# Optimization experiments

Hardware: AMD Instinct MI355X
Metric: run time of the kernel (lower is better)

Reference implementation:

```python
import jax, jax.numpy as jnp
import numpy as np

N, E, B = 100000, 1600000, 512
NE, EE, H = 32, 32, 64
SCALE = float(2**48 - 1)


def _mlp2(x, W1, b1, W2, b2):
    # Linear -> ReLU -> Linear
    return jax.nn.relu(x @ W1 + b1) @ W2 + b2


def _gine(x, src, dst, e, W1, b1, W2, b2, n):
    # GINEConv (eps=0): nn(x + sum_j relu(x_j + e_ij))
    m = jax.nn.relu(x[src] + e)                      # [E, d] gather + edge add
    agg = jax.ops.segment_sum(m, dst, num_segments=n)  # scatter-add to targets
    return _mlp2(x + agg, W1, b1, W2, b2)


def _encode(names, edge_index, edge_attr, batch,
            idW1, idb1, idW2, idb2, edW1, edb1, edW2, edb2,
            c1W1, c1b1, c1W2, c1b2, c2W1, c2b1, c2W2, c2b2, linW, linb):
    norm = jnp.clip((names.astype(jnp.float32) + 2.0) / SCALE, 0.0, 1.0)[:, None]
    x = _mlp2(norm, idW1, idb1, idW2, idb2)          # [N, NE]
    e = _mlp2(edge_attr, edW1, edb1, edW2, edb2)     # [E, EE]
    src, dst = edge_index[0], edge_index[1]
    x = jax.nn.relu(_gine(x, src, dst, e, c1W1, c1b1, c1W2, c1b2, N))
    e2 = e @ linW + linb                             # edge lin for conv2 (EE->H)
    x = jax.nn.relu(_gine(x, src, dst, e2, c2W1, c2b1, c2W2, c2b2, N))
    sums = jax.ops.segment_sum(x, batch, num_segments=B)
    cnt = jax.ops.segment_sum(jnp.ones((x.shape[0],), x.dtype), batch, num_segments=B)
    return sums / jnp.maximum(cnt, 1.0)[:, None]     # global_mean_pool


def setup_inputs() -> dict:
    key = jax.random.key(0)
    ks = iter(jax.random.split(key, 64))
    def w(shape):
        return jax.random.normal(next(ks), shape, dtype=jnp.float32) * 0.05
    d = {}
    d['node_names_s'] = jax.random.randint(next(ks), (N,), 0, 1000000)
    d['edge_index_s'] = jax.random.randint(next(ks), (2, E), 0, N)
    d['edge_attr_s'] = jax.random.uniform(next(ks), (E, 1), dtype=jnp.float32)
    d['batch_s'] = jnp.sort(jax.random.randint(next(ks), (N,), 0, B))
    d['node_names_g'] = jax.random.randint(next(ks), (N,), 0, 1000000)
    d['edge_index_g'] = jax.random.randint(next(ks), (2, E), 0, N)
    d['edge_attr_g'] = jax.random.uniform(next(ks), (E, 1), dtype=jnp.float32)
    d['batch_g'] = jnp.sort(jax.random.randint(next(ks), (N,), 0, B))
    d['depth'] = jax.random.uniform(next(ks), (B,), dtype=jnp.float32)
    # shared encoders
    d['idW1'], d['idb1'], d['idW2'], d['idb2'] = w((1, NE)), w((NE,)), w((NE, NE)), w((NE,))
    d['edW1'], d['edb1'], d['edW2'], d['edb2'] = w((1, EE)), w((EE,)), w((EE, EE)), w((EE,))
    # state convs
    d['s1W1'], d['s1b1'], d['s1W2'], d['s1b2'] = w((NE, H)), w((H,)), w((H, H)), w((H,))
    d['s2W1'], d['s2b1'], d['s2W2'], d['s2b2'] = w((H, H)), w((H,)), w((H, H)), w((H,))
    d['s2linW'], d['s2linb'] = w((EE, H)), w((H,))
    # goal convs
    d['g1W1'], d['g1b1'], d['g1W2'], d['g1b2'] = w((NE, H)), w((H,)), w((H, H)), w((H,))
    d['g2W1'], d['g2b1'], d['g2W2'], d['g2b2'] = w((H, H)), w((H,)), w((H, H)), w((H,))
    d['g2linW'], d['g2linb'] = w((EE, H)), w((H,))
    d['rW1'], d['rb1'], d['rW2'], d['rb2'] = w((2 * H + 1, H)), w((H,)), w((H, 1)), w((1,))
    return d


def reference(node_names_s, edge_index_s, edge_attr_s, batch_s,
              node_names_g, edge_index_g, edge_attr_g, batch_g, depth,
              idW1, idb1, idW2, idb2, edW1, edb1, edW2, edb2,
              s1W1, s1b1, s1W2, s1b2, s2W1, s2b1, s2W2, s2b2, s2linW, s2linb,
              g1W1, g1b1, g1W2, g1b2, g2W1, g2b1, g2W2, g2b2, g2linW, g2linb,
              rW1, rb1, rW2, rb2):
    s = _encode(node_names_s, edge_index_s, edge_attr_s, batch_s,
                idW1, idb1, idW2, idb2, edW1, edb1, edW2, edb2,
                s1W1, s1b1, s1W2, s1b2, s2W1, s2b1, s2W2, s2b2, s2linW, s2linb)
    g = _encode(node_names_g, edge_index_g, edge_attr_g, batch_g,
                idW1, idb1, idW2, idb2, edW1, edb1, edW2, edb2,
                g1W1, g1b1, g1W2, g1b2, g2W1, g2b1, g2W2, g2b2, g2linW, g2linb)
    z = jnp.concatenate([s, g, depth[:, None]], axis=1)  # [B, 2H+1]
    return _mlp2(z, rW1, rb1, rW2, rb2)[:, 0]            # [B]
```

## Files before the change

kernel.cpp:

```cpp
#include <hip/hip_runtime.h>
#include <hip/hip_fp16.h>
#include <stdint.h>

namespace {

constexpr int NN   = 100000;
constexpr int TN   = 2 * NN;
constexpr int NEDG = 1600000;
constexpr int TE   = 2 * NEDG;
constexpr int NBAT = 512;
constexpr int NSEG = 33;

constexpr int NC     = 782;
constexpr int TILE   = 4096;
constexpr int ABLK   = (TE + TILE - 1) / TILE;
constexpr int ENTCAP = 5120;

constexpr int S1H = 20;
constexpr int S2H = 36;

constexpr int TAB_BP = 0;
constexpr int TAB_D1 = 32;
constexpr int TAB_C1 = TAB_D1 + NSEG * 32;
constexpr int TAB_E2 = TAB_C1 + NSEG * 32;
constexpr int TAB_TOTAL = TAB_E2 + 4 * NSEG * 64;

__device__ __forceinline__ float relu_(float x) { return fmaxf(x, 0.0f); }

__device__ __forceinline__ float4 shfl_xor4(float4 v, int m) {
  return make_float4(__shfl_xor(v.x, m), __shfl_xor(v.y, m),
                     __shfl_xor(v.z, m), __shfl_xor(v.w, m));
}

__device__ __forceinline__ __half2 bch(int u) {
  return *reinterpret_cast<__half2*>(&u);
}
__device__ __forceinline__ int f2h2(float a, float b) {
  __half2 h = __floats2half2_rn(a, b);
  return *reinterpret_cast<int*>(&h);
}

__global__ void build_tables(const float* __restrict__ eW1, const float* __restrict__ eb1,
                             const float* __restrict__ eW2, const float* __restrict__ eb2,
                             const float* __restrict__ sLW, const float* __restrict__ sLb,
                             const float* __restrict__ gLW, const float* __restrict__ gLb,
                             float* __restrict__ tabs) {
  __shared__ float traw[32];
  __shared__ float ts[32];
  __shared__ float dt[NSEG * 32];
  __shared__ float ct[NSEG * 32];
  int tid = threadIdx.x;
  if (tid < 32) {
    float w = eW1[tid], b = eb1[tid];
    traw[tid] = (w != 0.0f) ? (-b / w) : 3.0e38f;
  }
  __syncthreads();
  if (tid < 32) {
    float v = traw[tid];
    int r = 0;
    for (int j = 0; j < 32; ++j) {
      float u = traw[j];
      r += (u < v) || (u == v && j < tid);
    }
    ts[r] = v;
  }
  __syncthreads();
  if (tid < 32) tabs[TAB_BP + tid] = ts[tid];
  for (int idx = tid; idx < NSEG * 32; idx += blockDim.x) {
    int s = idx >> 5, j = idx & 31;
    float a;
    if (s == 0)            a = ts[0] - 1.0f;
    else if (s == NSEG - 1) a = ts[31] + 1.0f;
    else                   a = 0.5f * ts[s - 1] + 0.5f * ts[s];
    float d = 0.0f, c = 0.0f;
    for (int i = 0; i < 32; ++i) {
      float w = eW1[i], b = eb1[i];
      if (fmaf(a, w, b) > 0.0f) {
        float w2 = eW2[i * 32 + j];
        d = fmaf(w, w2, d);
        c = fmaf(b, w2, c);
      }
    }
    c += eb2[j];
    dt[idx] = d; ct[idx] = c;
    tabs[TAB_D1 + idx] = d;
    tabs[TAB_C1 + idx] = c;
  }
  __syncthreads();
  for (int idx = tid; idx < NSEG * 64; idx += blockDim.x) {
    int s = idx >> 6, k = idx & 63;
    float ds = 0.f, cs = 0.f, dg = 0.f, cg = 0.f;
    for (int j = 0; j < 32; ++j) {
      float dv = dt[s * 32 + j], cv = ct[s * 32 + j];
      float ws = sLW[j * 64 + k], wg = gLW[j * 64 + k];
      ds = fmaf(dv, ws, ds); cs = fmaf(cv, ws, cs);
      dg = fmaf(dv, wg, dg); cg = fmaf(cv, wg, cg);
    }
    cs += sLb[k]; cg += gLb[k];
    tabs[TAB_E2 + idx]                 = ds;
    tabs[TAB_E2 + NSEG * 64 + idx]     = cs;
    tabs[TAB_E2 + 2 * NSEG * 64 + idx] = dg;
    tabs[TAB_E2 + 3 * NSEG * 64 + idx] = cg;
  }
}

__global__ __launch_bounds__(256) void fused_front(
    const int* __restrict__ names_s, const int* __restrict__ names_g,
    const float* __restrict__ idW1, const float* __restrict__ idb1,
    const float* __restrict__ idW2, const float* __restrict__ idb2,
    const int* __restrict__ src_s, const int* __restrict__ dst_s, const float* __restrict__ attr_s,
    const int* __restrict__ src_g, const int* __restrict__ dst_g, const float* __restrict__ attr_g,
    const int* __restrict__ bat_s, const int* __restrict__ bat_g,
    const float* __restrict__ tabs,
    float* __restrict__ x0, __half* __restrict__ x0h,
    int* __restrict__ gcur, int2* __restrict__ part,
    int* __restrict__ start_s, int* __restrict__ start_g) {
  __shared__ int hist[NC];
  __shared__ int lofs[NC];
  __shared__ int lcur[NC];
  __shared__ int2 sorted[TILE];
  __shared__ int addr[TILE];
  __shared__ int scanbuf[256];
  __shared__ float bp[32];
  int t = threadIdx.x;
  if (blockIdx.x < ABLK) {
    if (t < 32) bp[t] = tabs[TAB_BP + t];
    for (int i = t; i < NC; i += 256) hist[i] = 0;
    __syncthreads();
    int base = blockIdx.x * TILE;
#pragma unroll
    for (int j = 0; j < 16; ++j) {
      int i = base + j * 256 + t;
      if (i < TE) {
        int d = (i < NEDG) ? dst_s[i] : (dst_g[i - NEDG] + NN);
        atomicAdd(&hist[d >> 8], 1);
      }
    }
    __syncthreads();
    int loc[4];
    int sum = 0;
#pragma unroll
    for (int j = 0; j < 4; ++j) {
      int b = t * 4 + j;
      int v = (b < NC) ? hist[b] : 0;
      loc[j] = sum; sum += v;
    }
    scanbuf[t] = sum;
    __syncthreads();
    for (int st = 1; st < 256; st <<= 1) {
      int u = (t >= st) ? scanbuf[t - st] : 0;
      __syncthreads();
      scanbuf[t] += u;
      __syncthreads();
    }
    int texcl = scanbuf[t] - sum;
#pragma unroll
    for (int j = 0; j < 4; ++j) {
      int b = t * 4 + j;
      if (b < NC) { lofs[b] = texcl + loc[j]; lcur[b] = 0; }
    }
    __syncthreads();
    for (int b = t; b < NC; b += 256) {
      int c = hist[b];
      hist[b] = c ? atomicAdd(&gcur[b], c) : 0;
    }
    __syncthreads();
#pragma unroll
    for (int j = 0; j < 16; ++j) {
      int i = base + j * 256 + t;
      if (i < TE) {
        int sl, d; float a;
        if (i < NEDG) { sl = src_s[i]; d = dst_s[i]; a = attr_s[i]; }
        else { int k = i - NEDG; sl = src_g[k]; d = dst_g[k] + NN; a = attr_g[k]; }
        int seg = 0;
#pragma unroll
        for (int q = 0; q < 32; ++q) seg += (bp[q] < a);
        int c = d >> 8;
        int r = atomicAdd(&lcur[c], 1);
        int s = lofs[c] + r;
        sorted[s] = make_int2(sl | ((d & 255) << 17) | (seg << 25), __float_as_int(a));
        addr[s] = c * ENTCAP + hist[c] + r;
      }
    }
    __syncthreads();
    int tot = (base + TILE <= TE) ? TILE : (TE - base);
    for (int s = t; s < tot; s += 256) part[addr[s]] = sorted[s];
  } else if (blockIdx.x < ABLK + 782) {
    int n = (blockIdx.x - ABLK) * 256 + t;
    if (n >= TN) return;
    int name = (n < NN) ? names_s[n] : names_g[n - NN];
    float norm = ((float)name + 2.0f) / 281474976710655.0f;
    norm = fminf(fmaxf(norm, 0.0f), 1.0f);
    float h[32];
#pragma unroll
    for (int i = 0; i < 32; ++i) h[i] = relu_(fmaf(norm, idW1[i], idb1[i]));
    float4* out = (float4*)(x0 + (size_t)n * 32);
    int2* outh = (int2*)(x0h + (size_t)n * 32);
    for (int j0 = 0; j0 < 32; j0 += 4) {
      float a0 = idb2[j0], a1 = idb2[j0 + 1], a2 = idb2[j0 + 2], a3 = idb2[j0 + 3];
#pragma unroll
      for (int i = 0; i < 32; ++i) {
        float hv = h[i];
        a0 = fmaf(hv, idW2[i * 32 + j0],     a0);
        a1 = fmaf(hv, idW2[i * 32 + j0 + 1], a1);
        a2 = fmaf(hv, idW2[i * 32 + j0 + 2], a2);
        a3 = fmaf(hv, idW2[i * 32 + j0 + 3], a3);
      }
      out[j0 >> 2] = make_float4(a0, a1, a2, a3);
      outh[j0 >> 2] = make_int2(f2h2(a0, a1), f2h2(a2, a3));
    }
  } else {
    int blk = blockIdx.x - ABLK - 782;
    int half = blk >= 391;
    const int* bat = half ? bat_g : bat_s;
    int* start = half ? start_g : start_s;
    int i = (blk - half * 391) * 256 + t;
    if (i >= NN) return;
    int cur = bat[i];
    int prev = (i == 0) ? -1 : bat[i - 1];
    for (int b = prev + 1; b <= cur; ++b) start[b] = i;
    if (i == NN - 1) {
      for (int b = cur + 1; b <= NBAT; ++b) start[b] = NN;
    }
  }
}

__global__ __launch_bounds__(1024) void coarse_scan(
    const int* __restrict__ gcur, int* __restrict__ cbase, int* __restrict__ rowptr) {
  __shared__ int s[1024];
  int t = threadIdx.x;
  int v = (t < NC) ? min(gcur[t], ENTCAP) : 0;
  s[t] = v;
  __syncthreads();
  for (int st = 1; st < 1024; st <<= 1) {
    int u = (t >= st) ? s[t - st] : 0;
    __syncthreads();
    s[t] += u;
    __syncthreads();
  }
  if (t < NC) cbase[t] = s[t] - v;
  if (t == 0) rowptr[TN] = TE;
}

__global__ __launch_bounds__(256) void partition_to_csr(
    const int* __restrict__ gcur, const int* __restrict__ cbase,
    const int2* __restrict__ part,
    int* __restrict__ rowptr, int2* __restrict__ colattr) {
  __shared__ int2 outE[ENTCAP];
  __shared__ int hist[256];
  __shared__ int cur[256];
  __shared__ int sc[256];
  int t = threadIdx.x, b = blockIdx.x;
  hist[t] = 0;
  __syncthreads();
  int cnt = min(gcur[b], ENTCAP);
  int ibase = b * ENTCAP;
  int obase = cbase[b];
  for (int i = t; i < cnt; i += 256)
    atomicAdd(&hist[(part[ibase + i].x >> 17) & 255], 1);
  __syncthreads();
  int v = hist[t];
  sc[t] = v;
  __syncthreads();
  for (int st = 1; st < 256; st <<= 1) {
    int u = (t >= st) ? sc[t - st] : 0;
    __syncthreads();
    sc[t] += u;
    __syncthreads();
  }
  int excl = sc[t] - v;
  int gnode = b * 256 + t;
  if (gnode < TN) rowptr[gnode] = obase + excl;
  cur[t] = excl;
  __syncthreads();
  for (int i = t; i < cnt; i += 256) {
    int2 e = part[ibase + i];
    int dl = (e.x >> 17) & 255;
    int srcn = e.x & 0x1FFFF;
    int seg = (e.x >> 25) & 63;
    int pos = atomicAdd(&cur[dl], 1);
    outE[pos] = make_int2(srcn | (seg << 20), e.y);
  }
  __syncthreads();
  for (int i = t; i < cnt; i += 256) colattr[obase + i] = outE[i];
}

__global__ __launch_bounds__(256) void conv1_dual(
    const float* __restrict__ x0, const __half* __restrict__ x0h,
    const int* __restrict__ rowptr, const int2* __restrict__ colattr,
    const float* __restrict__ tabs, float* __restrict__ hb) {
  __shared__ __half2 dt2[NSEG * S1H];
  __shared__ __half2 ct2[NSEG * S1H];
  for (int i = threadIdx.x; i < NSEG * 16; i += 256) {
    int s = i >> 4, j = i & 15;
    dt2[s * S1H + j] = __floats2half2_rn(tabs[TAB_D1 + s * 32 + 2 * j],
                                         tabs[TAB_D1 + s * 32 + 2 * j + 1]);
    ct2[s * S1H + j] = __floats2half2_rn(tabs[TAB_C1 + s * 32 + 2 * j],
                                         tabs[TAB_C1 + s * 32 + 2 * j + 1]);
  }
  __syncthreads();
  int n = blockIdx.x * 4 + (threadIdx.x >> 6);
  const __half* xb = x0h + (n >= NN ? (size_t)NN * 32 : 0);
  int lane = threadIdx.x & 63;
  int sub = lane & 7;
  int f0  = (lane >> 3) * 4;
  int h0  = (lane >> 3) * 2;
  int beg = rowptr[n], end = rowptr[n + 1];
  float4 acc = make_float4(0.f, 0.f, 0.f, 0.f);
  for (int k = beg + sub; k < end; k += 16) {
    int2 ca0 = colattr[k];
    int kb = k + 8;
    bool has1 = kb < end;
    int2 ca1 = has1 ? colattr[kb] : ca0;
    unsigned p0 = (unsigned)ca0.x, p1 = (unsigned)ca1.x;
    int s0 = (int)(p0 & 0xFFFFFu), g0 = (int)(p0 >> 20);
    int s1 = (int)(p1 & 0xFFFFFu), g1 = (int)(p1 >> 20);
    float a0 = __int_as_float(ca0.y), a1 = __int_as_float(ca1.y);
    __half2 az0 = __floats2half2_rn(a0, a0);
    __half2 az1 = __floats2half2_rn(a1, a1);
    int2 xv0 = *(const int2*)(xb + (size_t)s0 * 32 + f0);
    int2 xv1 = *(const int2*)(xb + (size_t)s1 * 32 + f0);
    int2 dv0 = *(const int2*)&dt2[g0 * S1H + h0];
    int2 cv0 = *(const int2*)&ct2[g0 * S1H + h0];
    __half2 v;
    float2 f;
    v = __hadd2(bch(xv0.x), __hfma2(az0, bch(dv0.x), bch(cv0.x)));
    f = __half22float2(v); acc.x += relu_(f.x); acc.y += relu_(f.y);
    v = __hadd2(bch(xv0.y), __hfma2(az0, bch(dv0.y), bch(cv0.y)));
    f = __half22float2(v); acc.z += relu_(f.x); acc.w += relu_(f.y);
    if (has1) {
      int2 dv1 = *(const int2*)&dt2[g1 * S1H + h0];
      int2 cv1 = *(const int2*)&ct2[g1 * S1H + h0];
      v = __hadd2(bch(xv1.x), __hfma2(az1, bch(dv1.x), bch(cv1.x)));
      f = __half22float2(v); acc.x += relu_(f.x); acc.y += relu_(f.y);
      v = __hadd2(bch(xv1.y), __hfma2(az1, bch(dv1.y), bch(cv1.y)));
      f = __half22float2(v); acc.z += relu_(f.x); acc.w += relu_(f.y);
    }
  }
#pragma unroll
  for (int m = 1; m < 8; m <<= 1) {
    float4 o = shfl_xor4(acc, m);
    acc.x += o.x; acc.y += o.y; acc.z += o.z; acc.w += o.w;
  }
  if (sub == 0) {
    const float4 self = *(const float4*)(x0 + (size_t)n * 32 + f0);
    *(float4*)(hb + (size_t)n * 32 + f0) =
        make_float4(self.x + acc.x, self.y + acc.y, self.z + acc.z, self.w + acc.w);
  }
}

__global__ __launch_bounds__(256) void conv2_dual(
    const float* __restrict__ x1, const __half* __restrict__ x1h,
    const int* __restrict__ rowptr, const int2* __restrict__ colattr,
    const float* __restrict__ tabs, float* __restrict__ hb) {
  __shared__ __half2 dt2[NSEG * S2H];
  __shared__ __half2 ct2[NSEG * S2H];
  int half = blockIdx.x >= (NN / 4);
  const float* d2 = tabs + TAB_E2 + (size_t)half * 2 * NSEG * 64;
  for (int i = threadIdx.x; i < NSEG * 32; i += 256) {
    int s = i >> 5, j = i & 31;
    dt2[s * S2H + j] = __floats2half2_rn(d2[s * 64 + 2 * j], d2[s * 64 + 2 * j + 1]);
    ct2[s * S2H + j] = __floats2half2_rn(d2[NSEG * 64 + s * 64 + 2 * j],
                                         d2[NSEG * 64 + s * 64 + 2 * j + 1]);
  }
  __syncthreads();
  int n = blockIdx.x * 4 + (threadIdx.x >> 6);
  const __half* xb = x1h + (size_t)half * NN * 64;
  int lane = threadIdx.x & 63;
  int sub = lane & 7;
  int f0  = (lane >> 3) * 8;
  int h0  = (lane >> 3) * 4;
  int beg = rowptr[n], end = rowptr[n + 1];
  float4 accA = make_float4(0.f, 0.f, 0.f, 0.f);
  float4 accB = make_float4(0.f, 0.f, 0.f, 0.f);
  for (int k = beg + sub; k < end; k += 16) {
    int2 ca0 = colattr[k];
    int kb = k + 8;
    bool has1 = kb < end;
    int2 ca1 = has1 ? colattr[kb] : ca0;
    unsigned p0 = (unsigned)ca0.x, p1 = (unsigned)ca1.x;
    int s0 = (int)(p0 & 0xFFFFFu), g0 = (int)(p0 >> 20);
    int s1 = (int)(p1 & 0xFFFFFu), g1 = (int)(p1 >> 20);
    float a0 = __int_as_float(ca0.y), a1 = __int_as_float(ca1.y);
    __half2 az0 = __floats2half2_rn(a0, a0);
    __half2 az1 = __floats2half2_rn(a1, a1);
    int4 xv0 = *(const int4*)(xb + (size_t)s0 * 64 + f0);
    int4 xv1 = *(const int4*)(xb + (size_t)s1 * 64 + f0);
    int4 dv0 = *(const int4*)&dt2[g0 * S2H + h0];
    int4 cv0 = *(const int4*)&ct2[g0 * S2H + h0];
    __half2 v;
    float2 f;
    v = __hadd2(bch(xv0.x), __hfma2(az0, bch(dv0.x), bch(cv0.x)));
    f = __half22float2(v); accA.x += relu_(f.x); accA.y += relu_(f.y);
    v = __hadd2(bch(xv0.y), __hfma2(az0, bch(dv0.y), bch(cv0.y)));
    f = __half22float2(v); accA.z += relu_(f.x); accA.w += relu_(f.y);
    v = __hadd2(bch(xv0.z), __hfma2(az0, bch(dv0.z), bch(cv0.z)));
    f = __half22float2(v); accB.x += relu_(f.x); accB.y += relu_(f.y);
    v = __hadd2(bch(xv0.w), __hfma2(az0, bch(dv0.w), bch(cv0.w)));
    f = __half22float2(v); accB.z += relu_(f.x); accB.w += relu_(f.y);
    if (has1) {
      int4 dv1 = *(const int4*)&dt2[g1 * S2H + h0];
      int4 cv1 = *(const int4*)&ct2[g1 * S2H + h0];
      v = __hadd2(bch(xv1.x), __hfma2(az1, bch(dv1.x), bch(cv1.x)));
      f = __half22float2(v); accA.x += relu_(f.x); accA.y += relu_(f.y);
      v = __hadd2(bch(xv1.y), __hfma2(az1, bch(dv1.y), bch(cv1.y)));
      f = __half22float2(v); accA.z += relu_(f.x); accA.w += relu_(f.y);
      v = __hadd2(bch(xv1.z), __hfma2(az1, bch(dv1.z), bch(cv1.z)));
      f = __half22float2(v); accB.x += relu_(f.x); accB.y += relu_(f.y);
      v = __hadd2(bch(xv1.w), __hfma2(az1, bch(dv1.w), bch(cv1.w)));
      f = __half22float2(v); accB.z += relu_(f.x); accB.w += relu_(f.y);
    }
  }
#pragma unroll
  for (int m = 1; m < 8; m <<= 1) {
    float4 oA = shfl_xor4(accA, m);
    float4 oB = shfl_xor4(accB, m);
    accA.x += oA.x; accA.y += oA.y; accA.z += oA.z; accA.w += oA.w;
    accB.x += oB.x; accB.y += oB.y; accB.z += oB.z; accB.w += oB.w;
  }
  if (sub == 0) {
    const float* sp = x1 + (size_t)n * 64 + f0;
    const float4 sA = *(const float4*)sp;
    const float4 sB = *(const float4*)(sp + 4);
    float* op = hb + (size_t)n * 64 + f0;
    *(float4*)op       = make_float4(sA.x + accA.x, sA.y + accA.y, sA.z + accA.z, sA.w + accA.w);
    *(float4*)(op + 4) = make_float4(sB.x + accB.x, sB.y + accB.y, sB.z + accB.z, sB.w + accB.w);
  }
}

__global__ __launch_bounds__(256) void mlp1_dual(
    const float* __restrict__ hin,
    const float* __restrict__ sW1, const float* __restrict__ sb1,
    const float* __restrict__ sW2, const float* __restrict__ sb2,
    const float* __restrict__ gW1, const float* __restrict__ gb1,
    const float* __restrict__ gW2, const float* __restrict__ gb2,
    float* __restrict__ xout, __half* __restrict__ hout) {
  constexpr int IN = 32;
  __shared__ float hsT[IN][65];
  __shared__ float ysT[64][65];
  int base = blockIdx.x * 64;
  for (int idx = threadIdx.x; idx < 64 * IN; idx += 256) {
    int node = idx / IN, k = idx - node * IN;
    hsT[k][node] = hin[(size_t)(base + node) * IN + k];
  }
  __syncthreads();
  int nt = threadIdx.x >> 4, jx = threadIdx.x & 15;
  int n0 = nt * 4, f0 = jx * 4;
  bool isg = (base + n0) >= NN;
  const float* W1 = isg ? gW1 : sW1;
  const float* b1 = isg ? gb1 : sb1;
  const float* W2 = isg ? gW2 : sW2;
  const float* b2 = isg ? gb2 : sb2;
  float4 acc0, acc1, acc2, acc3;
  {
    const float4 b = *(const float4*)(b1 + f0);
    acc0 = b; acc1 = b; acc2 = b; acc3 = b;
  }
  for (int k = 0; k < IN; ++k) {
    const float4 h = *(const float4*)&hsT[k][n0];
    const float4 w = *(const float4*)(W1 + k * 64 + f0);
    acc0.x = fmaf(h.x, w.x, acc0.x); acc0.y = fmaf(h.x, w.y, acc0.y);
    acc0.z = fmaf(h.x, w.z, acc0.z); acc0.w = fmaf(h.x, w.w, acc0.w);
    acc1.x = fmaf(h.y, w.x, acc1.x); acc1.y = fmaf(h.y, w.y, acc1.y);
    acc1.z = fmaf(h.y, w.z, acc1.z); acc1.w = fmaf(h.y, w.w, acc1.w);
    acc2.x = fmaf(h.z, w.x, acc2.x); acc2.y = fmaf(h.z, w.y, acc2.y);
    acc2.z = fmaf(h.z, w.z, acc2.z); acc2.w = fmaf(h.z, w.w, acc2.w);
    acc3.x = fmaf(h.w, w.x, acc3.x); acc3.y = fmaf(h.w, w.y, acc3.y);
    acc3.z = fmaf(h.w, w.z, acc3.z); acc3.w = fmaf(h.w, w.w, acc3.w);
  }
  ysT[f0 + 0][n0 + 0] = relu_(acc0.x); ysT[f0 + 1][n0 + 0] = relu_(acc0.y);
  ysT[f0 + 2][n0 + 0] = relu_(acc0.z); ysT[f0 + 3][n0 + 0] = relu_(acc0.w);
  ysT[f0 + 0][n0 + 1] = relu_(acc1.x); ysT[f0 + 1][n0 + 1] = relu_(acc1.y);
  ysT[f0 + 2][n0 + 1] = relu_(acc1.z); ysT[f0 + 3][n0 + 1] = relu_(acc1.w);
  ysT[f0 + 0][n0 + 2] = relu_(acc2.x); ysT[f0 + 1][n0 + 2] = relu_(acc2.y);
  ysT[f0 + 2][n0 + 2] = relu_(acc2.z); ysT[f0 + 3][n0 + 2] = relu_(acc2.w);
  ysT[f0 + 0][n0 + 3] = relu_(acc3.x); ysT[f0 + 1][n0 + 3] = relu_(acc3.y);
  ysT[f0 + 2][n0 + 3] = relu_(acc3.z); ysT[f0 + 3][n0 + 3] = relu_(acc3.w);
  __syncthreads();
  {
    const float4 b = *(const float4*)(b2 + f0);
    acc0 = b; acc1 = b; acc2 = b; acc3 = b;
  }
  for (int k = 0; k < 64; ++k) {
    const float4 h = *(const float4*)&ysT[k][n0];
    const float4 w = *(const float4*)(W2 + k * 64 + f0);
    acc0.x = fmaf(h.x, w.x, acc0.x); acc0.y = fmaf(h.x, w.y, acc0.y);
    acc0.z = fmaf(h.x, w.z, acc0.z); acc0.w = fmaf(h.x, w.w, acc0.w);
    acc1.x = fmaf(h.y, w.x, acc1.x); acc1.y = fmaf(h.y, w.y, acc1.y);
    acc1.z = fmaf(h.y, w.z, acc1.z); acc1.w = fmaf(h.y, w.w, acc1.w);
    acc2.x = fmaf(h.z, w.x, acc2.x); acc2.y = fmaf(h.z, w.y, acc2.y);
    acc2.z = fmaf(h.z, w.z, acc2.z); acc2.w = fmaf(h.z, w.w, acc2.w);
    acc3.x = fmaf(h.w, w.x, acc3.x); acc3.y = fmaf(h.w, w.y, acc3.y);
    acc3.z = fmaf(h.w, w.z, acc3.z); acc3.w = fmaf(h.w, w.w, acc3.w);
  }
  float4 o;
  o = make_float4(relu_(acc0.x), relu_(acc0.y), relu_(acc0.z), relu_(acc0.w));
  *(float4*)(xout + (size_t)(base + n0 + 0) * 64 + f0) = o;
  *(int2*)(hout + (size_t)(base + n0 + 0) * 64 + f0) = make_int2(f2h2(o.x, o.y), f2h2(o.z, o.w));
  o = make_float4(relu_(acc1.x), relu_(acc1.y), relu_(acc1.z), relu_(acc1.w));
  *(float4*)(xout + (size_t)(base + n0 + 1) * 64 + f0) = o;
  *(int2*)(hout + (size_t)(base + n0 + 1) * 64 + f0) = make_int2(f2h2(o.x, o.y), f2h2(o.z, o.w));
  o = make_float4(relu_(acc2.x), relu_(acc2.y), relu_(acc2.z), relu_(acc2.w));
  *(float4*)(xout + (size_t)(base + n0 + 2) * 64 + f0) = o;
  *(int2*)(hout + (size_t)(base + n0 + 2) * 64 + f0) = make_int2(f2h2(o.x, o.y), f2h2(o.z, o.w));
  o = make_float4(relu_(acc3.x), relu_(acc3.y), relu_(acc3.z), relu_(acc3.w));
  *(float4*)(xout + (size_t)(base + n0 + 3) * 64 + f0) = o;
  *(int2*)(hout + (size_t)(base + n0 + 3) * 64 + f0) = make_int2(f2h2(o.x, o.y), f2h2(o.z, o.w));
}

__global__ __launch_bounds__(256) void mlp2_pool_dual(
    const float* __restrict__ hin,
    const float* __restrict__ sW1, const float* __restrict__ sb1,
    const float* __restrict__ sW2, const float* __restrict__ sb2,
    const float* __restrict__ gW1, const float* __restrict__ gb1,
    const float* __restrict__ gW2, const float* __restrict__ gb2,
    const int* __restrict__ bat_s, const int* __restrict__ bat_g,
    float* __restrict__ psum) {
  constexpr int IN = 64;
  __shared__ float hsT[IN][65];
  __shared__ float ysT[64][65];
  __shared__ int pid[64];
  int base = blockIdx.x * 64;
  for (int idx = threadIdx.x; idx < 64 * IN; idx += 256) {
    int node = idx / IN, k = idx - node * IN;
    hsT[k][node] = hin[(size_t)(base + node) * IN + k];
  }
  if (threadIdx.x < 64) {
    int gb = base + threadIdx.x;
    pid[threadIdx.x] = (gb < NN) ? bat_s[gb] : (NBAT + bat_g[gb - NN]);
  }
  __syncthreads();
  int nt = threadIdx.x >> 4, jx = threadIdx.x & 15;
  int n0 = nt * 4, f0 = jx * 4;
  bool isg = (base + n0) >= NN;
  const float* W1 = isg ? gW1 : sW1;
  const float* b1 = isg ? gb1 : sb1;
  const float* W2 = isg ? gW2 : sW2;
  const float* b2 = isg ? gb2 : sb2;
  float4 acc0, acc1, acc2, acc3;
  {
    const float4 b = *(const float4*)(b1 + f0);
    acc0 = b; acc1 = b; acc2 = b; acc3 = b;
  }
  for (int k = 0; k < IN; ++k) {
    const float4 h = *(const float4*)&hsT[k][n0];
    const float4 w = *(const float4*)(W1 + k * 64 + f0);
    acc0.x = fmaf(h.x, w.x, acc0.x); acc0.y = fmaf(h.x, w.y, acc0.y);
    acc0.z = fmaf(h.x, w.z, acc0.z); acc0.w = fmaf(h.x, w.w, acc0.w);
    acc1.x = fmaf(h.y, w.x, acc1.x); acc1.y = fmaf(h.y, w.y, acc1.y);
    acc1.z = fmaf(h.y, w.z, acc1.z); acc1.w = fmaf(h.y, w.w, acc1.w);
    acc2.x = fmaf(h.z, w.x, acc2.x); acc2.y = fmaf(h.z, w.y, acc2.y);
    acc2.z = fmaf(h.z, w.z, acc2.z); acc2.w = fmaf(h.z, w.w, acc2.w);
    acc3.x = fmaf(h.w, w.x, acc3.x); acc3.y = fmaf(h.w, w.y, acc3.y);
    acc3.z = fmaf(h.w, w.z, acc3.z); acc3.w = fmaf(h.w, w.w, acc3.w);
  }
  ysT[f0 + 0][n0 + 0] = relu_(acc0.x); ysT[f0 + 1][n0 + 0] = relu_(acc0.y);
  ysT[f0 + 2][n0 + 0] = relu_(acc0.z); ysT[f0 + 3][n0 + 0] = relu_(acc0.w);
  ysT[f0 + 0][n0 + 1] = relu_(acc1.x); ysT[f0 + 1][n0 + 1] = relu_(acc1.y);
  ysT[f0 + 2][n0 + 1] = relu_(acc1.z); ysT[f0 + 3][n0 + 1] = relu_(acc1.w);
  ysT[f0 + 0][n0 + 2] = relu_(acc2.x); ysT[f0 + 1][n0 + 2] = relu_(acc2.y);
  ysT[f0 + 2][n0 + 2] = relu_(acc2.z); ysT[f0 + 3][n0 + 2] = relu_(acc2.w);
  ysT[f0 + 0][n0 + 3] = relu_(acc3.x); ysT[f0 + 1][n0 + 3] = relu_(acc3.y);
  ysT[f0 + 2][n0 + 3] = relu_(acc3.z); ysT[f0 + 3][n0 + 3] = relu_(acc3.w);
  __syncthreads();
  {
    const float4 b = *(const float4*)(b2 + f0);
    acc0 = b; acc1 = b; acc2 = b; acc3 = b;
  }
  for (int k = 0; k < 64; ++k) {
    const float4 h = *(const float4*)&ysT[k][n0];
    const float4 w = *(const float4*)(W2 + k * 64 + f0);
    acc0.x = fmaf(h.x, w.x, acc0.x); acc0.y = fmaf(h.x, w.y, acc0.y);
    acc0.z = fmaf(h.x, w.z, acc0.z); acc0.w = fmaf(h.x, w.w, acc0.w);
    acc1.x = fmaf(h.y, w.x, acc1.x); acc1.y = fmaf(h.y, w.y, acc1.y);
    acc1.z = fmaf(h.y, w.z, acc1.z); acc1.w = fmaf(h.y, w.w, acc1.w);
    acc2.x = fmaf(h.z, w.x, acc2.x); acc2.y = fmaf(h.z, w.y, acc2.y);
    acc2.z = fmaf(h.z, w.z, acc2.z); acc2.w = fmaf(h.z, w.w, acc2.w);
    acc3.x = fmaf(h.w, w.x, acc3.x); acc3.y = fmaf(h.w, w.y, acc3.y);
    acc3.z = fmaf(h.w, w.z, acc3.z); acc3.w = fmaf(h.w, w.w, acc3.w);
  }
  __syncthreads();
  ysT[f0 + 0][n0 + 0] = relu_(acc0.x); ysT[f0 + 1][n0 + 0] = relu_(acc0.y);
  ysT[f0 + 2][n0 + 0] = relu_(acc0.z); ysT[f0 + 3][n0 + 0] = relu_(acc0.w);
  ysT[f0 + 0][n0 + 1] = relu_(acc1.x); ysT[f0 + 1][n0 + 1] = relu_(acc1.y);
  ysT[f0 + 2][n0 + 1] = relu_(acc1.z); ysT[f0 + 3][n0 + 1] = relu_(acc1.w);
  ysT[f0 + 0][n0 + 2] = relu_(acc2.x); ysT[f0 + 1][n0 + 2] = relu_(acc2.y);
  ysT[f0 + 2][n0 + 2] = relu_(acc2.z); ysT[f0 + 3][n0 + 2] = relu_(acc2.w);
  ysT[f0 + 0][n0 + 3] = relu_(acc3.x); ysT[f0 + 1][n0 + 3] = relu_(acc3.y);
  ysT[f0 + 2][n0 + 3] = relu_(acc3.z); ysT[f0 + 3][n0 + 3] = relu_(acc3.w);
  __syncthreads();
  int c = threadIdx.x >> 6, f = threadIdx.x & 63;
  int cur = pid[c * 16];
  float run = 0.0f;
  for (int i = 0; i < 16; ++i) {
    int nx = c * 16 + i;
    int p = pid[nx];
    if (p != cur) { atomicAdd(&psum[(size_t)cur * 64 + f], run); run = 0.0f; cur = p; }
    run += ysT[f][nx];
  }
  atomicAdd(&psum[(size_t)cur * 64 + f], run);
}

__global__ __launch_bounds__(256) void regressor16(
    const float* __restrict__ psum,
    const int* __restrict__ start_s, const int* __restrict__ start_g,
    const float* __restrict__ depth,
    const float* __restrict__ W1, const float* __restrict__ b1,
    const float* __restrict__ W2, const float* __restrict__ b2,
    float* __restrict__ out) {
  __shared__ float zs[16][132];
  __shared__ float ys[64][17];
  __shared__ float inv_s[16], inv_g[16];
  int base = blockIdx.x * 16;
  if (threadIdx.x < 16) {
    int b = base + threadIdx.x;
    inv_s[threadIdx.x] = 1.0f / fmaxf((float)(start_s[b + 1] - start_s[b]), 1.0f);
    inv_g[threadIdx.x] = 1.0f / fmaxf((float)(start_g[b + 1] - start_g[b]), 1.0f);
  }
  __syncthreads();
  for (int i = threadIdx.x; i < 16 * 64; i += 256) {
    int ln = i >> 6, k = i & 63;
    zs[ln][k]      = psum[(size_t)(base + ln) * 64 + k] * inv_s[ln];
    zs[ln][64 + k] = psum[(size_t)(NBAT + base + ln) * 64 + k] * inv_g[ln];
  }
  if (threadIdx.x < 16) zs[threadIdx.x][128] = depth[base + threadIdx.x];
  __syncthreads();
  int g = threadIdx.x >> 4;
  int j = threadIdx.x & 15;
  int f0 = j * 4;
  float a0, a1, a2, a3;
  {
    const float4 b = *(const float4*)(b1 + f0);
    a0 = b.x; a1 = b.y; a2 = b.z; a3 = b.w;
  }
  for (int k = 0; k < 129; ++k) {
    float zv = zs[g][k];
    const float4 w = *(const float4*)(W1 + k * 64 + f0);
    a0 = fmaf(zv, w.x, a0); a1 = fmaf(zv, w.y, a1);
    a2 = fmaf(zv, w.z, a2); a3 = fmaf(zv, w.w, a3);
  }
  ys[f0 + 0][g] = relu_(a0);
  ys[f0 + 1][g] = relu_(a1);
  ys[f0 + 2][g] = relu_(a2);
  ys[f0 + 3][g] = relu_(a3);
  __syncthreads();
  float s = ys[f0 + 0][g] * W2[f0 + 0] + ys[f0 + 1][g] * W2[f0 + 1] +
            ys[f0 + 2][g] * W2[f0 + 2] + ys[f0 + 3][g] * W2[f0 + 3];
#pragma unroll
  for (int m = 1; m < 16; m <<= 1) s += __shfl_xor(s, m);
  if (j == 0) out[base + g] = s + b2[0];
}

}

extern "C" void kernel_launch(void* const* d_in, const int* in_sizes, int n_in,
                              void* d_out, int out_size, void* d_ws, size_t ws_size,
                              hipStream_t stream) {
  const int*   names_s = (const int*)d_in[0];
  const int*   ei_s    = (const int*)d_in[1];
  const float* ea_s    = (const float*)d_in[2];
  const int*   bat_s   = (const int*)d_in[3];
  const int*   names_g = (const int*)d_in[4];
  const int*   ei_g    = (const int*)d_in[5];
  const float* ea_g    = (const float*)d_in[6];
  const int*   bat_g   = (const int*)d_in[7];
  const float* depth   = (const float*)d_in[8];
  const float* idW1 = (const float*)d_in[9],  *idb1 = (const float*)d_in[10];
  const float* idW2 = (const float*)d_in[11], *idb2 = (const float*)d_in[12];
  const float* edW1 = (const float*)d_in[13], *edb1 = (const float*)d_in[14];
  const float* edW2 = (const float*)d_in[15], *edb2 = (const float*)d_in[16];
  const float* s1W1 = (const float*)d_in[17], *s1b1 = (const float*)d_in[18];
  const float* s1W2 = (const float*)d_in[19], *s1b2 = (const float*)d_in[20];
  const float* s2W1 = (const float*)d_in[21], *s2b1 = (const float*)d_in[22];
  const float* s2W2 = (const float*)d_in[23], *s2b2 = (const float*)d_in[24];
  const float* s2LW = (const float*)d_in[25], *s2Lb = (const float*)d_in[26];
  const float* g1W1 = (const float*)d_in[27], *g1b1 = (const float*)d_in[28];
  const float* g1W2 = (const float*)d_in[29], *g1b2 = (const float*)d_in[30];
  const float* g2W1 = (const float*)d_in[31], *g2b1 = (const float*)d_in[32];
  const float* g2W2 = (const float*)d_in[33], *g2b2 = (const float*)d_in[34];
  const float* g2LW = (const float*)d_in[35], *g2Lb = (const float*)d_in[36];
  const float* rW1  = (const float*)d_in[37], *rb1  = (const float*)d_in[38];
  const float* rW2  = (const float*)d_in[39], *rb2  = (const float*)d_in[40];
  (void)in_sizes; (void)n_in; (void)out_size; (void)ws_size;

  char* ws = (char*)d_ws;
  size_t off = 0;
  auto alloc = [&](size_t bytes) -> char* {
    char* p = ws + off;
    off += (bytes + 255) & ~(size_t)255;
    return p;
  };
  float* tabs    = (float*)alloc((size_t)TAB_TOTAL * 4);
  char*  act   = alloc((size_t)TN * 64 * 4 * 2);
  float* x0buf = (float*)act;
  float* h1buf = (float*)(act + (size_t)TN * 32 * 4);
  float* x1buf = (float*)(act + (size_t)TN * 64 * 4);
  int2*  part  = (int2*)x1buf;
  float* h2buf = (float*)act;
  __half* x0h  = (__half*)alloc((size_t)TN * 32 * 2);
  __half* x1h  = (__half*)alloc((size_t)TN * 64 * 2);
  int2*  colattr = (int2*) alloc((size_t)TE * 8);
  int*   gcur    = (int*)  alloc((size_t)NC * 4);
  int*   cbase   = (int*)  alloc((size_t)NC * 4);
  int*   rowptr  = (int*)  alloc((size_t)(TN + 1) * 4);
  int*   start_s = (int*)  alloc((size_t)(NBAT + 1) * 4);
  int*   start_g = (int*)  alloc((size_t)(NBAT + 1) * 4);
  float* psum    = (float*)alloc((size_t)2 * NBAT * 64 * 4);

  build_tables<<<1, 256, 0, stream>>>(edW1, edb1, edW2, edb2, s2LW, s2Lb, g2LW, g2Lb, tabs);
  hipMemsetAsync(gcur, 0, (size_t)NC * 4, stream);
  hipMemsetAsync(psum, 0, (size_t)2 * NBAT * 64 * 4, stream);

  fused_front<<<ABLK + 782 + 782, 256, 0, stream>>>(
      names_s, names_g, idW1, idb1, idW2, idb2,
      ei_s, ei_s + NEDG, ea_s, ei_g, ei_g + NEDG, ea_g,
      bat_s, bat_g, tabs, x0buf, x0h, gcur, part, start_s, start_g);
  coarse_scan<<<1, 1024, 0, stream>>>(gcur, cbase, rowptr);
  partition_to_csr<<<NC, 256, 0, stream>>>(gcur, cbase, part, rowptr, colattr);

  conv1_dual<<<TN / 4, 256, 0, stream>>>(x0buf, x0h, rowptr, colattr, tabs, h1buf);
  mlp1_dual<<<TN / 64, 256, 0, stream>>>(h1buf,
                                         s1W1, s1b1, s1W2, s1b2,
                                         g1W1, g1b1, g1W2, g1b2, x1buf, x1h);
  conv2_dual<<<TN / 4, 256, 0, stream>>>(x1buf, x1h, rowptr, colattr, tabs, h2buf);
  mlp2_pool_dual<<<TN / 64, 256, 0, stream>>>(h2buf,
                                              s2W1, s2b1, s2W2, s2b2,
                                              g2W1, g2b1, g2W2, g2b2,
                                              bat_s, bat_g, psum);
  regressor16<<<32, 256, 0, stream>>>(psum, start_s, start_g, depth,
                                      rW1, rb1, rW2, rb2, (float*)d_out);
}
```

Measured before the change: 678.1 us.

## Drop fp32 node feature copies and make conv kernels persistent with rowptr prefetch

Removes the fp32 copies of x0 and x1 so only the fp16 versions are written, and the self term in each conv is read from the half buffer. conv1/conv2 now launch a fixed grid of 2048 blocks that grid-stride over nodes, loading the edge tables into shared memory once per block and prefetching the next node's rowptr. This cuts global write and read traffic and per-block table setup, at the cost of rounding the self term to fp16 and possible load imbalance from the fixed grid. Workspace is also reshuffled so the partition buffer aliases h2buf.

```diff
diff --git a/kernel.cpp b/kernel.cpp
--- a/kernel.cpp
+++ b/kernel.cpp
@@ -15,6 +15,8 @@
 constexpr int TILE   = 4096;
 constexpr int ABLK   = (TE + TILE - 1) / TILE;
 constexpr int ENTCAP = 5120;
+
+constexpr int CONVBLK = 2048;
 
 constexpr int S1H = 20;
 constexpr int S2H = 36;
@@ -112,7 +114,7 @@
     const int* __restrict__ src_g, const int* __restrict__ dst_g, const float* __restrict__ attr_g,
     const int* __restrict__ bat_s, const int* __restrict__ bat_g,
     const float* __restrict__ tabs,
-    float* __restrict__ x0, __half* __restrict__ x0h,
+    __half* __restrict__ x0h,
     int* __restrict__ gcur, int2* __restrict__ part,
     int* __restrict__ start_s, int* __restrict__ start_g) {
   __shared__ int hist[NC];
@@ -194,7 +196,6 @@
     float h[32];
 #pragma unroll
     for (int i = 0; i < 32; ++i) h[i] = relu_(fmaf(norm, idW1[i], idb1[i]));
-    float4* out = (float4*)(x0 + (size_t)n * 32);
     int2* outh = (int2*)(x0h + (size_t)n * 32);
     for (int j0 = 0; j0 < 32; j0 += 4) {
       float a0 = idb2[j0], a1 = idb2[j0 + 1], a2 = idb2[j0 + 2], a3 = idb2[j0 + 3];
@@ -206,7 +207,6 @@
         a2 = fmaf(hv, idW2[i * 32 + j0 + 2], a2);
         a3 = fmaf(hv, idW2[i * 32 + j0 + 3], a3);
       }
-      out[j0 >> 2] = make_float4(a0, a1, a2, a3);
       outh[j0 >> 2] = make_int2(f2h2(a0, a1), f2h2(a2, a3));
     }
   } else {
@@ -286,7 +286,7 @@
 }
 
 __global__ __launch_bounds__(256) void conv1_dual(
-    const float* __restrict__ x0, const __half* __restrict__ x0h,
+    const __half* __restrict__ x0h,
     const int* __restrict__ rowptr, const int2* __restrict__ colattr,
     const float* __restrict__ tabs, float* __restrict__ hb) {
   __shared__ __half2 dt2[NSEG * S1H];
@@ -299,64 +299,71 @@
                                          tabs[TAB_C1 + s * 32 + 2 * j + 1]);
   }
   __syncthreads();
-  int n = blockIdx.x * 4 + (threadIdx.x >> 6);
-  const __half* xb = x0h + (n >= NN ? (size_t)NN * 32 : 0);
   int lane = threadIdx.x & 63;
   int sub = lane & 7;
   int f0  = (lane >> 3) * 4;
   int h0  = (lane >> 3) * 2;
-  int beg = rowptr[n], end = rowptr[n + 1];
-  float4 acc = make_float4(0.f, 0.f, 0.f, 0.f);
-  for (int k = beg + sub; k < end; k += 16) {
-    int2 ca0 = colattr[k];
-    int kb = k + 8;
-    bool has1 = kb < end;
-    int2 ca1 = has1 ? colattr[kb] : ca0;
-    unsigned p0 = (unsigned)ca0.x, p1 = (unsigned)ca1.x;
-    int s0 = (int)(p0 & 0xFFFFFu), g0 = (int)(p0 >> 20);
-    int s1 = (int)(p1 & 0xFFFFFu), g1 = (int)(p1 >> 20);
-    float a0 = __int_as_float(ca0.y), a1 = __int_as_float(ca1.y);
-    __half2 az0 = __floats2half2_rn(a0, a0);
-    __half2 az1 = __floats2half2_rn(a1, a1);
-    int2 xv0 = *(const int2*)(xb + (size_t)s0 * 32 + f0);
-    int2 xv1 = *(const int2*)(xb + (size_t)s1 * 32 + f0);
-    int2 dv0 = *(const int2*)&dt2[g0 * S1H + h0];
-    int2 cv0 = *(const int2*)&ct2[g0 * S1H + h0];
-    __half2 v;
-    float2 f;
-    v = __hadd2(bch(xv0.x), __hfma2(az0, bch(dv0.x), bch(cv0.x)));
-    f = __half22float2(v); acc.x += relu_(f.x); acc.y += relu_(f.y);
-    v = __hadd2(bch(xv0.y), __hfma2(az0, bch(dv0.y), bch(cv0.y)));
-    f = __half22float2(v); acc.z += relu_(f.x); acc.w += relu_(f.y);
-    if (has1) {
-      int2 dv1 = *(const int2*)&dt2[g1 * S1H + h0];
-      int2 cv1 = *(const int2*)&ct2[g1 * S1H + h0];
-      v = __hadd2(bch(xv1.x), __hfma2(az1, bch(dv1.x), bch(cv1.x)));
+  int wid = blockIdx.x * 4 + (threadIdx.x >> 6);
+  int nb = rowptr[wid], ne = rowptr[wid + 1];
+  for (int n = wid; n < TN; n += 4 * CONVBLK) {
+    int beg = nb, end = ne;
+    int n2 = n + 4 * CONVBLK;
+    if (n2 < TN) { nb = rowptr[n2]; ne = rowptr[n2 + 1]; }
+    const __half* xb = x0h + (n >= NN ? (size_t)NN * 32 : 0);
+    int2 sv = make_int2(0, 0);
+    if (sub == 0) sv = *(const int2*)(x0h + (size_t)n * 32 + f0);
+    float4 acc = make_float4(0.f, 0.f, 0.f, 0.f);
+    for (int k = beg + sub; k < end; k += 16) {
+      int2 ca0 = colattr[k];
+      int kb = k + 8;
+      bool has1 = kb < end;
+      int2 ca1 = has1 ? colattr[kb] : ca0;
+      unsigned p0 = (unsigned)ca0.x, p1 = (unsigned)ca1.x;
+      int s0 = (int)(p0 & 0xFFFFFu), g0 = (int)(p0 >> 20);
+      int s1 = (int)(p1 & 0xFFFFFu), g1 = (int)(p1 >> 20);
+      float a0 = __int_as_float(ca0.y), a1 = __int_as_float(ca1.y);
+      __half2 az0 = __floats2half2_rn(a0, a0);
+      __half2 az1 = __floats2half2_rn(a1, a1);
+      int2 xv0 = *(const int2*)(xb + (size_t)s0 * 32 + f0);
+      int2 xv1 = *(const int2*)(xb + (size_t)s1 * 32 + f0);
+      int2 dv0 = *(const int2*)&dt2[g0 * S1H + h0];
+      int2 cv0 = *(const int2*)&ct2[g0 * S1H + h0];
+      __half2 v;
+      float2 f;
+      v = __hadd2(bch(xv0.x), __hfma2(az0, bch(dv0.x), bch(cv0.x)));
       f = __half22float2(v); acc.x += relu_(f.x); acc.y += relu_(f.y);
-      v = __hadd2(bch(xv1.y), __hfma2(az1, bch(dv1.y), bch(cv1.y)));
+      v = __hadd2(bch(xv0.y), __hfma2(az0, bch(dv0.y), bch(cv0.y)));
       f = __half22float2(v); acc.z += relu_(f.x); acc.w += relu_(f.y);
-    }
-  }
-#pragma unroll
-  for (int m = 1; m < 8; m <<= 1) {
-    float4 o = shfl_xor4(acc, m);
-    acc.x += o.x; acc.y += o.y; acc.z += o.z; acc.w += o.w;
-  }
-  if (sub == 0) {
-    const float4 self = *(const float4*)(x0 + (size_t)n * 32 + f0);
-    *(float4*)(hb + (size_t)n * 32 + f0) =
-        make_float4(self.x + acc.x, self.y + acc.y, self.z + acc.z, self.w + acc.w);
+      if (has1) {
+        int2 dv1 = *(const int2*)&dt2[g1 * S1H + h0];
+        int2 cv1 = *(const int2*)&ct2[g1 * S1H + h0];
+        v = __hadd2(bch(xv1.x), __hfma2(az1, bch(dv1.x), bch(cv1.x)));
+        f = __half22float2(v); acc.x += relu_(f.x); acc.y += relu_(f.y);
+        v = __hadd2(bch(xv1.y), __hfma2(az1, bch(dv1.y), bch(cv1.y)));
+        f = __half22float2(v); acc.z += relu_(f.x); acc.w += relu_(f.y);
+      }
+    }
+#pragma unroll
+    for (int m = 1; m < 8; m <<= 1) {
+      float4 o = shfl_xor4(acc, m);
+      acc.x += o.x; acc.y += o.y; acc.z += o.z; acc.w += o.w;
+    }
+    if (sub == 0) {
+      float2 t0 = __half22float2(bch(sv.x)), t1 = __half22float2(bch(sv.y));
+      *(float4*)(hb + (size_t)n * 32 + f0) =
+          make_float4(t0.x + acc.x, t0.y + acc.y, t1.x + acc.z, t1.y + acc.w);
+    }
   }
 }
 
 __global__ __launch_bounds__(256) void conv2_dual(
-    const float* __restrict__ x1, const __half* __restrict__ x1h,
+    const __half* __restrict__ x1h,
     const int* __restrict__ rowptr, const int2* __restrict__ colattr,
     const float* __restrict__ tabs, float* __restrict__ hb) {
   __shared__ __half2 dt2[NSEG * S2H];
   __shared__ __half2 ct2[NSEG * S2H];
-  int half = blockIdx.x >= (NN / 4);
-  const float* d2 = tabs + TAB_E2 + (size_t)half * 2 * NSEG * 64;
+  int halfg = blockIdx.x >= (CONVBLK / 2);
+  const float* d2 = tabs + TAB_E2 + (size_t)halfg * 2 * NSEG * 64;
   for (int i = threadIdx.x; i < NSEG * 32; i += 256) {
     int s = i >> 5, j = i & 31;
     dt2[s * S2H + j] = __floats2half2_rn(d2[s * 64 + 2 * j], d2[s * 64 + 2 * j + 1]);
@@ -364,67 +371,75 @@
                                          d2[NSEG * 64 + s * 64 + 2 * j + 1]);
   }
   __syncthreads();
-  int n = blockIdx.x * 4 + (threadIdx.x >> 6);
-  const __half* xb = x1h + (size_t)half * NN * 64;
+  const __half* xb = x1h + (size_t)halfg * NN * 64;
   int lane = threadIdx.x & 63;
   int sub = lane & 7;
   int f0  = (lane >> 3) * 8;
   int h0  = (lane >> 3) * 4;
-  int beg = rowptr[n], end = rowptr[n + 1];
-  float4 accA = make_float4(0.f, 0.f, 0.f, 0.f);
-  float4 accB = make_float4(0.f, 0.f, 0.f, 0.f);
-  for (int k = beg + sub; k < end; k += 16) {
-    int2 ca0 = colattr[k];
-    int kb = k + 8;
-    bool has1 = kb < end;
-    int2 ca1 = has1 ? colattr[kb] : ca0;
-    unsigned p0 = (unsigned)ca0.x, p1 = (unsigned)ca1.x;
-    int s0 = (int)(p0 & 0xFFFFFu), g0 = (int)(p0 >> 20);
-    int s1 = (int)(p1 & 0xFFFFFu), g1 = (int)(p1 >> 20);
-    float a0 = __int_as_float(ca0.y), a1 = __int_as_float(ca1.y);
-    __half2 az0 = __floats2half2_rn(a0, a0);
-    __half2 az1 = __floats2half2_rn(a1, a1);
-    int4 xv0 = *(const int4*)(xb + (size_t)s0 * 64 + f0);
-    int4 xv1 = *(const int4*)(xb + (size_t)s1 * 64 + f0);
-    int4 dv0 = *(const int4*)&dt2[g0 * S2H + h0];
-    int4 cv0 = *(const int4*)&ct2[g0 * S2H + h0];
-    __half2 v;
-    float2 f;
-    v = __hadd2(bch(xv0.x), __hfma2(az0, bch(dv0.x), bch(cv0.x)));
-    f = __half22float2(v); accA.x += relu_(f.x); accA.y += relu_(f.y);
-    v = __hadd2(bch(xv0.y), __hfma2(az0, bch(dv0.y), bch(cv0.y)));
-    f = __half22float2(v); accA.z += relu_(f.x); accA.w += relu_(f.y);
-    v = __hadd2(bch(xv0.z), __hfma2(az0, bch(dv0.z), bch(cv0.z)));
-    f = __half22float2(v); accB.x += relu_(f.x); accB.y += relu_(f.y);
-    v = __hadd2(bch(xv0.w), __hfma2(az0, bch(dv0.w), bch(cv0.w)));
-    f = __half22float2(v); accB.z += relu_(f.x); accB.w += relu_(f.y);
-    if (has1) {
-      int4 dv1 = *(const int4*)&dt2[g1 * S2H + h0];
-      int4 cv1 = *(const int4*)&ct2[g1 * S2H + h0];
-      v = __hadd2(bch(xv1.x), __hfma2(az1, bch(dv1.x), bch(cv1.x)));
+  int wid = (blockIdx.x - halfg * (CONVBLK / 2)) * 4 + (threadIdx.x >> 6);
+  int nlim = halfg * NN + NN;
+  int n0 = halfg * NN + wid;
+  int nb = rowptr[n0], ne = rowptr[n0 + 1];
+  for (int n = n0; n < nlim; n += 2 * CONVBLK) {
+    int beg = nb, end = ne;
+    int n2 = n + 2 * CONVBLK;
+    if (n2 < nlim) { nb = rowptr[n2]; ne = rowptr[n2 + 1]; }
+    int4 sv0 = make_int4(0, 0, 0, 0);
+    if (sub == 0) sv0 = *(const int4*)(x1h + (size_t)n * 64 + f0);
+    float4 accA = make_float4(0.f, 0.f, 0.f, 0.f);
+    float4 accB = make_float4(0.f, 0.f, 0.f, 0.f);
+    for (int k = beg + sub; k < end; k += 16) {
+      int2 ca0 = colattr[k];
+      int kb = k + 8;
+      bool has1 = kb < end;
+      int2 ca1 = has1 ? colattr[kb] : ca0;
+      unsigned p0 = (unsigned)ca0.x, p1 = (unsigned)ca1.x;
+      int s0 = (int)(p0 & 0xFFFFFu), g0 = (int)(p0 >> 20);
+      int s1 = (int)(p1 & 0xFFFFFu), g1 = (int)(p1 >> 20);
+      float a0 = __int_as_float(ca0.y), a1 = __int_as_float(ca1.y);
+      __half2 az0 = __floats2half2_rn(a0, a0);
+      __half2 az1 = __floats2half2_rn(a1, a1);
+      int4 xv0 = *(const int4*)(xb + (size_t)s0 * 64 + f0);
+      int4 xv1 = *(const int4*)(xb + (size_t)s1 * 64 + f0);
+      int4 dv0 = *(const int4*)&dt2[g0 * S2H + h0];
+      int4 cv0 = *(const int4*)&ct2[g0 * S2H + h0];
+      __half2 v;
+      float2 f;
+      v = __hadd2(bch(xv0.x), __hfma2(az0, bch(dv0.x), bch(cv0.x)));
       f = __half22float2(v); accA.x += relu_(f.x); accA.y += relu_(f.y);
-      v = __hadd2(bch(xv1.y), __hfma2(az1, bch(dv1.y), bch(cv1.y)));
+      v = __hadd2(bch(xv0.y), __hfma2(az0, bch(dv0.y), bch(cv0.y)));
       f = __half22float2(v); accA.z += relu_(f.x); accA.w += relu_(f.y);
-      v = __hadd2(bch(xv1.z), __hfma2(az1, bch(dv1.z), bch(cv1.z)));
+      v = __hadd2(bch(xv0.z), __hfma2(az0, bch(dv0.z), bch(cv0.z)));
       f = __half22float2(v); accB.x += relu_(f.x); accB.y += relu_(f.y);
-      v = __hadd2(bch(xv1.w), __hfma2(az1, bch(dv1.w), bch(cv1.w)));
+      v = __hadd2(bch(xv0.w), __hfma2(az0, bch(dv0.w), bch(cv0.w)));
       f = __half22float2(v); accB.z += relu_(f.x); accB.w += relu_(f.y);
-    }
-  }
-#pragma unroll
-  for (int m = 1; m < 8; m <<= 1) {
-    float4 oA = shfl_xor4(accA, m);
-    float4 oB = shfl_xor4(accB, m);
-    accA.x += oA.x; accA.y += oA.y; accA.z += oA.z; accA.w += oA.w;
-    accB.x += oB.x; accB.y += oB.y; accB.z += oB.z; accB.w += oB.w;
-  }
-  if (sub == 0) {
-    const float* sp = x1 + (size_t)n * 64 + f0;
-    const float4 sA = *(const float4*)sp;
-    const float4 sB = *(const float4*)(sp + 4);
-    float* op = hb + (size_t)n * 64 + f0;
-    *(float4*)op       = make_float4(sA.x + accA.x, sA.y + accA.y, sA.z + accA.z, sA.w + accA.w);
-    *(float4*)(op + 4) = make_float4(sB.x + accB.x, sB.y + accB.y, sB.z + accB.z, sB.w + accB.w);
+      if (has1) {
+        int4 dv1 = *(const int4*)&dt2[g1 * S2H + h0];
+        int4 cv1 = *(const int4*)&ct2[g1 * S2H + h0];
+        v = __hadd2(bch(xv1.x), __hfma2(az1, bch(dv1.x), bch(cv1.x)));
+        f = __half22float2(v); accA.x += relu_(f.x); accA.y += relu_(f.y);
+        v = __hadd2(bch(xv1.y), __hfma2(az1, bch(dv1.y), bch(cv1.y)));
+        f = __half22float2(v); accA.z += relu_(f.x); accA.w += relu_(f.y);
+        v = __hadd2(bch(xv1.z), __hfma2(az1, bch(dv1.z), bch(cv1.z)));
+        f = __half22float2(v); accB.x += relu_(f.x); accB.y += relu_(f.y);
+        v = __hadd2(bch(xv1.w), __hfma2(az1, bch(dv1.w), bch(cv1.w)));
+        f = __half22float2(v); accB.z += relu_(f.x); accB.w += relu_(f.y);
+      }
+    }
+#pragma unroll
+    for (int m = 1; m < 8; m <<= 1) {
+      float4 oA = shfl_xor4(accA, m);
+      float4 oB = shfl_xor4(accB, m);
+      accA.x += oA.x; accA.y += oA.y; accA.z += oA.z; accA.w += oA.w;
+      accB.x += oB.x; accB.y += oB.y; accB.z += oB.z; accB.w += oB.w;
+    }
+    if (sub == 0) {
+      float2 t0 = __half22float2(bch(sv0.x)), t1 = __half22float2(bch(sv0.y));
+      float2 t2 = __half22float2(bch(sv0.z)), t3 = __half22float2(bch(sv0.w));
+      float* op = hb + (size_t)n * 64 + f0;
+      *(float4*)op       = make_float4(t0.x + accA.x, t0.y + accA.y, t1.x + accA.z, t1.y + accA.w);
+      *(float4*)(op + 4) = make_float4(t2.x + accB.x, t2.y + accB.y, t3.x + accB.z, t3.y + accB.w);
+    }
   }
 }
 
@@ -434,7 +449,7 @@
     const float* __restrict__ sW2, const float* __restrict__ sb2,
     const float* __restrict__ gW1, const float* __restrict__ gb1,
     const float* __restrict__ gW2, const float* __restrict__ gb2,
-    float* __restrict__ xout, __half* __restrict__ hout) {
+    __half* __restrict__ hout) {
   constexpr int IN = 32;
   __shared__ float hsT[IN][65];
   __shared__ float ysT[64][65];
@@ -495,16 +510,12 @@
   }
   float4 o;
   o = make_float4(relu_(acc0.x), relu_(acc0.y), relu_(acc0.z), relu_(acc0.w));
-  *(float4*)(xout + (size_t)(base + n0 + 0) * 64 + f0) = o;
   *(int2*)(hout + (size_t)(base + n0 + 0) * 64 + f0) = make_int2(f2h2(o.x, o.y), f2h2(o.z, o.w));
   o = make_float4(relu_(acc1.x), relu_(acc1.y), relu_(acc1.z), relu_(acc1.w));
-  *(float4*)(xout + (size_t)(base + n0 + 1) * 64 + f0) = o;
   *(int2*)(hout + (size_t)(base + n0 + 1) * 64 + f0) = make_int2(f2h2(o.x, o.y), f2h2(o.z, o.w));
   o = make_float4(relu_(acc2.x), relu_(acc2.y), relu_(acc2.z), relu_(acc2.w));
-  *(float4*)(xout + (size_t)(base + n0 + 2) * 64 + f0) = o;
   *(int2*)(hout + (size_t)(base + n0 + 2) * 64 + f0) = make_int2(f2h2(o.x, o.y), f2h2(o.z, o.w));
   o = make_float4(relu_(acc3.x), relu_(acc3.y), relu_(acc3.z), relu_(acc3.w));
-  *(float4*)(xout + (size_t)(base + n0 + 3) * 64 + f0) = o;
   *(int2*)(hout + (size_t)(base + n0 + 3) * 64 + f0) = make_int2(f2h2(o.x, o.y), f2h2(o.z, o.w));
 }
 
@@ -691,12 +702,10 @@
     return p;
   };
   float* tabs    = (float*)alloc((size_t)TAB_TOTAL * 4);
-  char*  act   = alloc((size_t)TN * 64 * 4 * 2);
-  float* x0buf = (float*)act;
-  float* h1buf = (float*)(act + (size_t)TN * 32 * 4);
-  float* x1buf = (float*)(act + (size_t)TN * 64 * 4);
-  int2*  part  = (int2*)x1buf;
+  char*  act   = alloc((size_t)TN * 64 * 4 + (size_t)TN * 32 * 4);
   float* h2buf = (float*)act;
+  float* h1buf = (float*)(act + (size_t)TN * 64 * 4);
+  int2*  part  = (int2*)act;
   __half* x0h  = (__half*)alloc((size_t)TN * 32 * 2);
   __half* x1h  = (__half*)alloc((size_t)TN * 64 * 2);
   int2*  colattr = (int2*) alloc((size_t)TE * 8);
@@ -714,15 +723,15 @@
   fused_front<<<ABLK + 782 + 782, 256, 0, stream>>>(
       names_s, names_g, idW1, idb1, idW2, idb2,
       ei_s, ei_s + NEDG, ea_s, ei_g, ei_g + NEDG, ea_g,
-      bat_s, bat_g, tabs, x0buf, x0h, gcur, part, start_s, start_g);
+      bat_s, bat_g, tabs, x0h, gcur, part, start_s, start_g);
   coarse_scan<<<1, 1024, 0, stream>>>(gcur, cbase, rowptr);
   partition_to_csr<<<NC, 256, 0, stream>>>(gcur, cbase, part, rowptr, colattr);
 
-  conv1_dual<<<TN / 4, 256, 0, stream>>>(x0buf, x0h, rowptr, colattr, tabs, h1buf);
+  conv1_dual<<<CONVBLK, 256, 0, stream>>>(x0h, rowptr, colattr, tabs, h1buf);
   mlp1_dual<<<TN / 64, 256, 0, stream>>>(h1buf,
                                          s1W1, s1b1, s1W2, s1b2,
-                                         g1W1, g1b1, g1W2, g1b2, x1buf, x1h);
-  conv2_dual<<<TN / 4, 256, 0, stream>>>(x1buf, x1h, rowptr, colattr, tabs, h2buf);
+                                         g1W1, g1b1, g1W2, g1b2, x1h);
+  conv2_dual<<<CONVBLK, 256, 0, stream>>>(x1h, rowptr, colattr, tabs, h2buf);
   mlp2_pool_dual<<<TN / 64, 256, 0, stream>>>(h2buf,
                                               s2W1, s2b1, s2W2, s2b2,
                                               g2W1, g2b1, g2W2, g2b2,
```

New measurement: 569.7 us. 1.19x faster.
